# Kernel tuning notes

Hardware: AMD Instinct MI355X
Metric: run time of the kernel (lower is better)

Reference implementation:

```python
import jax, jax.numpy as jnp
import numpy as np

S = 3072       # packed sequence length
DIM = 1280     # hidden dim
H = 16         # num heads
HD = DIM // H  # head dim = 80
NEG = -1e9     # additive mask value for cross-segment entries


def setup_inputs() -> dict:
    key = jax.random.key(0)
    ks = jax.random.split(key, 6)
    x = jax.random.normal(ks[0], (S, DIM), jnp.float32)
    # rope angle table [S, HD//2]
    rotary_pos_emb = jax.random.uniform(ks[1], (S, HD // 2), jnp.float32, 0.0, 2.0 * np.pi)
    # 4 equal image segments packed together
    cu_seqlens = jnp.array([0, 768, 1536, 2304, 3072], jnp.int32)
    w_qkv = jax.random.normal(ks[2], (3 * DIM, DIM), jnp.float32) * 0.02
    b_qkv = jax.random.normal(ks[3], (3 * DIM,), jnp.float32) * 0.02
    w_proj = jax.random.normal(ks[4], (DIM, DIM), jnp.float32) * 0.02
    b_proj = jax.random.normal(ks[5], (DIM,), jnp.float32) * 0.02
    return {"x": x, "cu_seqlens": cu_seqlens, "rotary_pos_emb": rotary_pos_emb,
            "w_qkv": w_qkv, "b_qkv": b_qkv, "w_proj": w_proj, "b_proj": b_proj}


def _rope(t, cos, sin):
    # t: [S, H, HD]; cos/sin: [S, 1, HD]
    t1, t2 = jnp.split(t, 2, axis=-1)
    rot = jnp.concatenate([-t2, t1], axis=-1)
    return t * cos + rot * sin


def reference(x, cu_seqlens, rotary_pos_emb, w_qkv, b_qkv, w_proj, b_proj):
    s, d = x.shape
    qkv = (x @ w_qkv.T + b_qkv).reshape(s, 3, H, HD)
    q, k, v = qkv[:, 0], qkv[:, 1], qkv[:, 2]  # each [S, H, HD]

    # NeoX-style rope with tiled (repeated) freqs, computed in fp32
    cos = jnp.cos(rotary_pos_emb)
    sin = jnp.sin(rotary_pos_emb)
    cos = jnp.concatenate([cos, cos], axis=-1)[:, None, :]  # [S,1,HD]
    sin = jnp.concatenate([sin, sin], axis=-1)[:, None, :]
    q = _rope(q.astype(jnp.float32), cos, sin).astype(x.dtype)
    k = _rope(k.astype(jnp.float32), cos, sin).astype(x.dtype)

    # block-diagonal varlen mask from cu_seqlens: segment id per position
    seg = jnp.searchsorted(cu_seqlens, jnp.arange(s), side='right') - 1  # [S]
    mask = jnp.where(seg[:, None] == seg[None, :], 0.0, NEG).astype(x.dtype)  # [S,S]

    scale = 1.0 / np.sqrt(HD).astype(np.float32)
    scores = jnp.einsum('qhd,khd->hqk', q, k) * scale + mask[None]  # [H,S,S]
    attn = jax.nn.softmax(scores, axis=-1)
    out = jnp.einsum('hqk,khd->qhd', attn, v).reshape(s, d)  # [S, DIM]
    return out @ w_proj.T + b_proj
```

## Files before the change

kernel.cpp:

```cpp
#include <hip/hip_runtime.h>


typedef __bf16 bf16;
typedef __bf16 bf16x4 __attribute__((ext_vector_type(4)));
typedef __bf16 bf16x8 __attribute__((ext_vector_type(8)));
typedef float f32x4 __attribute__((ext_vector_type(4)));
typedef float f32x16 __attribute__((ext_vector_type(16)));
typedef unsigned int u32;

constexpr int S = 3072;
constexpr int DIM = 1280;
constexpr int H = 16;
constexpr int HD = 80;
constexpr int KDP = 128;
constexpr int NQKV = 3 * DIM;

constexpr int MB_A = S / 256;
constexpr int NB_B = NQKV / 256;
constexpr int NKT = DIM / 32;

constexpr float QSCALE = 1.4426950408889634f / 8.94427190999916f;

__device__ __forceinline__ void gload_lds16(const void* g, void* l) {
  __builtin_amdgcn_global_load_lds(
      (const __attribute__((address_space(1))) void*)g,
      (__attribute__((address_space(3))) void*)l, 16, 0, 0);
}

__device__ __forceinline__ u32 pkbf2(float a, float b) {
  union { bf16 h[2]; u32 w; } u;
  u.h[0] = (bf16)a; u.h[1] = (bf16)b;
  return u.w;
}

__device__ __forceinline__ int swv(int s) {
  return ((((s >> 3) & 31) ^ ((s & 7) << 2)) << 2);
}

constexpr long PA_CHUNKS = (long)MB_A * NKT * 1024;
constexpr long PB_CHUNKS = (long)NB_B * NKT * 1024;
constexpr long PW_CHUNKS = (long)DIM * DIM / 8;
constexpr long KP_CHUNKS = (long)H * S * 48 / 8;
constexpr long CS_CHUNKS = (long)S * 40 / 8;
constexpr long TOT_CHUNKS = PA_CHUNKS + PB_CHUNKS + PW_CHUNKS + KP_CHUNKS + CS_CHUNKS;

__global__ __launch_bounds__(256) void pack_inputs(
    const float* __restrict__ x, const float* __restrict__ wq,
    const float* __restrict__ wp, const float* __restrict__ rope,
    bf16* __restrict__ pA, bf16* __restrict__ pB, bf16* __restrict__ wp16,
    bf16* __restrict__ Kb, float* __restrict__ ctab, float* __restrict__ stab) {
  long t = (long)blockIdx.x * 256 + threadIdx.x;
  if (t < PA_CHUNKS + PB_CHUNKS) {
    int blk, rem;
    const float* base;
    bf16* obase;
    bool isB = false;
    if (t < PA_CHUNKS) {
      blk = (int)(t / (NKT * 1024)); rem = (int)(t % (NKT * 1024));
      base = x; obase = pA + t * 8;
    } else {
      long t2 = t - PA_CHUNKS;
      blk = (int)(t2 / (NKT * 1024)); rem = (int)(t2 % (NKT * 1024));
      base = wq; obase = pB + t2 * 8;
      isB = true;
    }
    const int kt = rem >> 10, c = rem & 1023;
    const int lin = c * 16;
    const int logi = lin ^ (((lin >> 7) & 7) << 4);
    int row = logi >> 6;
    const int col = (logi & 63) >> 1;
    int grow = blk * 256 + row;
    if (isB && grow < 2560) {
      const int ty = grow / 1280, rm = grow % 1280;
      const int h = rm / 80, p = rm % 80;
      grow = ty * 1280 + h * 80 + (p >> 1) + (p & 1) * 40;
    }
    const float* src = base + (size_t)grow * DIM + kt * 32 + col;
    float4 v0 = *(const float4*)src;
    float4 v1 = *(const float4*)(src + 4);
    bf16x8 o = {(bf16)v0.x, (bf16)v0.y, (bf16)v0.z, (bf16)v0.w,
                (bf16)v1.x, (bf16)v1.y, (bf16)v1.z, (bf16)v1.w};
    *(bf16x8*)obase = o;
  } else if (t < PA_CHUNKS + PB_CHUNKS + PW_CHUNKS) {
    long t2 = t - PA_CHUNKS - PB_CHUNKS;
    const float* src = wp + t2 * 8;
    float4 v0 = *(const float4*)src;
    float4 v1 = *(const float4*)(src + 4);
    bf16x8 o = {(bf16)v0.x, (bf16)v0.y, (bf16)v0.z, (bf16)v0.w,
                (bf16)v1.x, (bf16)v1.y, (bf16)v1.z, (bf16)v1.w};
    *(bf16x8*)(wp16 + t2 * 8) = o;
  } else if (t < PA_CHUNKS + PB_CHUNKS + PW_CHUNKS + KP_CHUNKS) {
    long t2 = t - PA_CHUNKS - PB_CHUNKS - PW_CHUNKS;
    const int h = (int)(t2 / (S * 6)), r = (int)(t2 % (S * 6));
    const int s = r / 6, cc = r % 6;
    bf16x8 z = {};
    *(bf16x8*)(Kb + ((size_t)h * S + s) * KDP + 80 + cc * 8) = z;
  } else {
    long t3 = t - PA_CHUNKS - PB_CHUNKS - PW_CHUNKS - KP_CHUNKS;
#pragma unroll
    for (int k = 0; k < 8; k++) {
      const int idx = (int)(t3 * 8 + k);
      const int s = idx / 40, a = idx % 40;
      float sn, cs;
      __sincosf(rope[idx], &sn, &cs);
      ctab[a * S + s] = cs;
      stab[a * S + s] = sn;
    }
  }
}

__global__ __launch_bounds__(512, 2) void gemm256(
    const bf16* __restrict__ pA, const bf16* __restrict__ pB,
    const float* __restrict__ bias, const float* __restrict__ ctab,
    const float* __restrict__ stab, bf16* __restrict__ Qb,
    bf16* __restrict__ Kb, bf16* __restrict__ VTb) {
  extern __shared__ char lds[];
  const int tid = threadIdx.x;
  const int w = tid >> 6, lane = tid & 63;
  const int r15 = lane & 15, b4 = lane >> 4;
  const int wr = w >> 2, wc = w & 3;
  const int nwg = gridDim.x * gridDim.y;
  const int orig = blockIdx.y * gridDim.x + blockIdx.x;
  const int xcd = orig % 8, loc = orig / 8;
  const int qq = nwg / 8, rq = nwg % 8;
  const int swzid =
      (xcd < rq ? xcd * (qq + 1) : rq * (qq + 1) + (xcd - rq) * qq) + loc;
  const int nb = swzid % gridDim.x, mb = swzid / gridDim.x;
  const int m0 = mb * 256;
  const char* aPanel = (const char*)pA + (size_t)mb * NKT * 16384;
  const char* bPanel = (const char*)pB + (size_t)nb * NKT * 16384;
  auto stageA = [&](int kt) {
    char* s = lds + (kt & 3) * 32768;
    const char* g = aPanel + (size_t)kt * 16384;
    gload_lds16(g + tid * 16, s + tid * 16);
    gload_lds16(g + 8192 + tid * 16, s + 8192 + tid * 16);
  };
  auto stageB = [&](int kt) {
    char* s = lds + (kt & 3) * 32768 + 16384;
    const char* g = bPanel + (size_t)kt * 16384;
    gload_lds16(g + tid * 16, s + tid * 16);
    gload_lds16(g + 8192 + tid * 16, s + 8192 + tid * 16);
  };
  f32x4 acc[8][4] = {};
  stageA(0); stageB(0); stageA(1); stageB(1); stageA(2); stageB(2);
  asm volatile("s_waitcnt vmcnt(8)" ::: "memory");
  __builtin_amdgcn_s_barrier();
  for (int kt = 0; kt < NKT; ++kt) {
    const char* As = lds + (kt & 3) * 32768;
    const char* Bs = As + 16384;
    const bool pf = (kt + 3 < NKT);
    bf16x8 afr[4], bfr[4];
#pragma unroll
    for (int i = 0; i < 4; i++) {
      int a = (wr * 128 + i * 16 + r15) * 64 + b4 * 16;
      a ^= ((a >> 7) & 7) << 4;
      afr[i] = *(const bf16x8*)(As + a);
    }
#pragma unroll
    for (int j = 0; j < 4; j++) {
      int a = (wc * 64 + j * 16 + r15) * 64 + b4 * 16;
      a ^= ((a >> 7) & 7) << 4;
      bfr[j] = *(const bf16x8*)(Bs + a);
    }
    if (pf) stageA(kt + 3);
    asm volatile("" ::: "memory");
    __builtin_amdgcn_s_barrier();
    __builtin_amdgcn_s_setprio(1);
#pragma unroll
    for (int i = 0; i < 4; i++)
#pragma unroll
      for (int j = 0; j < 4; j++)
        acc[i][j] = __builtin_amdgcn_mfma_f32_16x16x32_bf16(afr[i], bfr[j],
                                                            acc[i][j], 0, 0, 0);
    __builtin_amdgcn_s_setprio(0);
    asm volatile("" ::: "memory");
    __builtin_amdgcn_s_barrier();
#pragma unroll
    for (int i = 0; i < 4; i++) {
      int a = (wr * 128 + 64 + i * 16 + r15) * 64 + b4 * 16;
      a ^= ((a >> 7) & 7) << 4;
      afr[i] = *(const bf16x8*)(As + a);
    }
    if (pf) stageB(kt + 3);
    asm volatile("" ::: "memory");
    __builtin_amdgcn_s_barrier();
    __builtin_amdgcn_s_setprio(1);
#pragma unroll
    for (int i = 0; i < 4; i++)
#pragma unroll
      for (int j = 0; j < 4; j++)
        acc[4 + i][j] = __builtin_amdgcn_mfma_f32_16x16x32_bf16(
            afr[i], bfr[j], acc[4 + i][j], 0, 0, 0);
    __builtin_amdgcn_s_setprio(0);
    const int rem = NKT - 2 - kt;
    if (rem >= 2)      asm volatile("s_waitcnt vmcnt(8)" ::: "memory");
    else if (rem == 1) asm volatile("s_waitcnt vmcnt(4)" ::: "memory");
    else if (rem == 0) asm volatile("s_waitcnt vmcnt(0)" ::: "memory");
    else               asm volatile("" ::: "memory");
    __builtin_amdgcn_s_barrier();
  }
  const int n0 = nb * 256;
  const int type = n0 / 1280;
  const int cpart0 = n0 - type * 1280;
  if (type < 2) {
#pragma unroll
    for (int j = 0; j < 4; j++) {
      const int c = wc * 64 + j * 16 + r15;
      const int cp = cpart0 + c;
      const int h = cp / 80, p = cp % 80;
      const int d = (p >> 1) + (p & 1) * 40;
      const float bv = bias[type * 1280 + h * 80 + d];
      const int a = p >> 1;
#pragma unroll
      for (int i = 0; i < 8; i++) {
        const int sl = wr * 128 + i * 16 + b4 * 4;
        f32x4 cs4 = *(const f32x4*)&ctab[a * S + m0 + sl];
        f32x4 sn4 = *(const f32x4*)&stab[a * S + m0 + sl];
#pragma unroll
        for (int r = 0; r < 4; r++) {
          float v = acc[i][j][r] + bv;
          float ov = __shfl_xor(v, 1);
          float res = (p & 1) ? (v * cs4[r] + ov * sn4[r])
                              : (v * cs4[r] - ov * sn4[r]);
          if (type == 0) res *= QSCALE;
          *(bf16*)(lds + (sl + r) * 512 + ((2 * c) ^ (((sl + r) & 7) << 4))) =
              (bf16)res;
        }
      }
    }
    __syncthreads();
#pragma unroll
    for (int t = 0; t < 16; t++) {
      const int task = t * 512 + tid;
      const int sl = task >> 5, c = (task & 31) * 8;
      bf16x8 v = *(const bf16x8*)(lds + sl * 512 + ((2 * c) ^ ((sl & 7) << 4)));
      const int cp = cpart0 + c, h = cp / 80, p = cp % 80;
      bf16* dst = type ? Kb + ((size_t)h * S + m0 + sl) * KDP + p
                       : Qb + ((size_t)h * S + m0 + sl) * HD + p;
      *(bf16x8*)dst = v;
    }
  } else {
#pragma unroll
    for (int j = 0; j < 4; j++) {
      const int c = wc * 64 + j * 16 + r15;
      const float bv = bias[2560 + cpart0 + c];
#pragma unroll
      for (int i = 0; i < 8; i++) {
        const int sl = wr * 128 + i * 16 + b4 * 4;
#pragma unroll
        for (int r = 0; r < 4; r++) {
          *(bf16*)(lds + (sl + r) * 512 + ((2 * c) ^ swv(sl + r))) =
              (bf16)(acc[i][j][r] + bv);
        }
      }
    }
    __syncthreads();
#pragma unroll
    for (int t = 0; t < 16; t++) {
      const int task = t * 512 + tid;
      const int c = task >> 5, s0 = (task & 31) * 8;
      union { bf16 h[8]; bf16x8 v; } o;
#pragma unroll
      for (int e = 0; e < 8; e++)
        o.h[e] = *(const bf16*)(lds + (s0 + e) * 512 + ((2 * c) ^ swv(s0 + e)));
      const int cp = cpart0 + c, h = cp / 80, d = cp % 80;
      *(bf16x8*)(VTb + ((size_t)(h * 80 + d)) * S + m0 + s0) = o.v;
    }
  }
}

__global__ __launch_bounds__(256) void gemm_proj(
    const bf16* __restrict__ A, const bf16* __restrict__ B,
    const float* __restrict__ bias, float* __restrict__ Cout, int M, int N,
    int K) {
  __shared__ bf16 Al[2][64 * 32];
  __shared__ bf16 Bl[2][128 * 32];
  const int tid = threadIdx.x;
  const int w = tid >> 6, lane = tid & 63;
  const int r15 = lane & 15, b4 = lane >> 4;
  const int nwg = gridDim.x * gridDim.y;
  const int orig = blockIdx.y * gridDim.x + blockIdx.x;
  const int swzid = (orig & 7) * (nwg >> 3) + (orig >> 3);
  const int bx = swzid % gridDim.x, by = swzid / gridDim.x;
  const int m0 = by * 64, n0 = bx * 128;
  const int wm = (w >> 1) * 32, wn = (w & 1) * 64;
  f32x4 acc[2][4] = {};
  const int row0 = tid >> 2, ko0 = (tid & 3) * 8;
  const bf16* Ar = A + (size_t)(m0 + row0) * K + ko0;
  const bf16* Br0 = B + (size_t)(n0 + row0) * K + ko0;
  const bf16* Br1 = B + (size_t)(n0 + row0 + 64) * K + ko0;

  auto stage = [&](int buf, int k0) {
    gload_lds16(Ar + k0, (char*)Al[buf] + tid * 16);
    gload_lds16(Br0 + k0, (char*)Bl[buf] + tid * 16);
    gload_lds16(Br1 + k0, (char*)Bl[buf] + 4096 + tid * 16);
  };

  stage(0, 0);
  int cur = 0;
  for (int k0 = 0; k0 < K; k0 += 32) {
    __syncthreads();
    if (k0 + 32 < K) stage(cur ^ 1, k0 + 32);
    bf16x8 af[2], bfr[4];
#pragma unroll
    for (int i = 0; i < 2; i++)
      af[i] = *(const bf16x8*)((const char*)Al[cur] + (wm + i * 16 + r15) * 64 + b4 * 16);
#pragma unroll
    for (int j = 0; j < 4; j++)
      bfr[j] = *(const bf16x8*)((const char*)Bl[cur] + (wn + j * 16 + r15) * 64 + b4 * 16);
#pragma unroll
    for (int i = 0; i < 2; i++)
#pragma unroll
      for (int j = 0; j < 4; j++)
        acc[i][j] = __builtin_amdgcn_mfma_f32_16x16x32_bf16(af[i], bfr[j], acc[i][j], 0, 0, 0);
    cur ^= 1;
  }
#pragma unroll
  for (int j = 0; j < 4; j++) {
    const int n = n0 + wn + j * 16 + r15;
    const float bv = bias[n];
#pragma unroll
    for (int i = 0; i < 2; i++) {
      const int mr = m0 + wm + i * 16 + b4 * 4;
#pragma unroll
      for (int r = 0; r < 4; r++)
        Cout[(size_t)(mr + r) * N + n] = acc[i][j][r] + bv;
    }
  }
}

__global__ __launch_bounds__(256, 3) void attn_kern(
    const bf16* __restrict__ Qg, const bf16* __restrict__ Kg,
    const bf16* __restrict__ Vg, const int* __restrict__ cu, int nseg,
    bf16* __restrict__ Out) {
  __shared__ bf16 Kl[2][64 * 128];
  __shared__ bf16 Vl[2][80 * 64];
  const int tid = threadIdx.x, w = tid >> 6, lane = tid & 63;
  const int r31 = lane & 31, hi = lane >> 5;
  const int pair = w >> 1, qs = w & 1;
  const int pt = tid & 127;
  const int nwg = gridDim.x;
  const int orig = blockIdx.x;
  const int swzb = (orig & 7) * (nwg >> 3) + (orig >> 3);
  const int h = swzb / 48, qb = swzb % 48;
  const int q = qb * 64 + qs * 32 + r31;
  int sq = 0, eq = S, lo = 0, hik = S;
  {
    const int qlo = qb * 64, qhi = qb * 64 + 63;
#pragma unroll
    for (int i = 0; i < 8; i++) {
      if (i >= nseg) break;
      int a = cu[i], b = cu[i + 1];
      if (q >= a && q < b) { sq = a; eq = b; }
      if (qlo >= a && qlo < b) lo = a;
      if (qhi >= a && qhi < b) hik = b;
    }
  }
  bf16x8 qf[5];
  {
    const bf16* qrow = Qg + ((size_t)h * S + q) * HD + hi * 8;
#pragma unroll
    for (int kk = 0; kk < 5; kk++) qf[kk] = *(const bf16x8*)(qrow + kk * 16);
  }
  int kdst[8], ksrc[8], vdst[5], vsrc[5];
#pragma unroll
  for (int c = 0; c < 8; c++) {
    int lin = (c * 128 + pt) * 16;
    int row = lin >> 8, colb = (lin & 255) ^ ((row & 15) << 4);
    kdst[c] = lin; ksrc[c] = row * KDP + colb / 2;
  }
#pragma unroll
  for (int c = 0; c < 5; c++) {
    int lin = (c * 128 + pt) * 16;
    int row = lin >> 7, colb = (lin & 127) ^ ((row & 7) << 4);
    vdst[c] = lin; vsrc[c] = row * S + colb / 2;
  }
  const bf16* Kbase = Kg + (size_t)h * S * KDP;
  const bf16* Vbase = Vg + (size_t)h * HD * S;
  char* Klp = (char*)Kl[pair];
  char* Vlp = (char*)Vl[pair];
  auto stage = [&](int k0) {
#pragma unroll
    for (int c = 0; c < 8; c++)
      gload_lds16(Kbase + (size_t)k0 * KDP + ksrc[c], Klp + kdst[c]);
#pragma unroll
    for (int c = 0; c < 5; c++)
      gload_lds16(Vbase + vsrc[c] + k0, Vlp + vdst[c]);
  };
  f32x16 o0 = {}, o1 = {}, o2 = {};
  float m = -1e30f, l = 0.f;
  const int nt = (hik - lo) >> 6;
  const int nit = (nt + 1) >> 1;
  for (int i = 0; i < nit; ++i) {
    const int t = 2 * i + pair;
    const bool act = t < nt;
    const int k0 = lo + t * 64;
    __syncthreads();
    if (act) stage(k0);
    asm volatile("s_waitcnt vmcnt(0)" ::: "memory");
    __syncthreads();
    if (!act) continue;
    f32x16 st0 = {}, st1 = {};
    __builtin_amdgcn_s_setprio(1);
#pragma unroll
    for (int kk = 0; kk < 5; kk++) {
      const int colb = kk * 32 + hi * 16;
      bf16x8 kf0 = *(const bf16x8*)(Klp + r31 * 256 + (colb ^ ((r31 & 15) << 4)));
      bf16x8 kf1 = *(const bf16x8*)(Klp + (32 + r31) * 256 + (colb ^ ((r31 & 15) << 4)));
      st0 = __builtin_amdgcn_mfma_f32_32x32x16_bf16(kf0, qf[kk], st0, 0, 0, 0);
      st1 = __builtin_amdgcn_mfma_f32_32x32x16_bf16(kf1, qf[kk], st1, 0, 0, 0);
    }
    __builtin_amdgcn_s_setprio(0);
    float tm = -3e38f;
    if (k0 >= sq && k0 + 63 < eq) {
#pragma unroll
      for (int j = 0; j < 16; j++) {
        tm = fmaxf(tm, st0[j]);
        tm = fmaxf(tm, st1[j]);
      }
    } else {
#pragma unroll
      for (int j = 0; j < 16; j++) {
        const int crow = (j & 3) + 8 * (j >> 2) + 4 * hi;
        int key0 = k0 + crow, key1 = k0 + 32 + crow;
        st0[j] = (key0 >= sq && key0 < eq) ? st0[j] : -1e30f;
        st1[j] = (key1 >= sq && key1 < eq) ? st1[j] : -1e30f;
        tm = fmaxf(tm, st0[j]);
        tm = fmaxf(tm, st1[j]);
      }
    }
    tm = fmaxf(tm, __shfl_xor(tm, 32));
    if (!__all(tm <= m + 8.f)) {
      const float mn = fmaxf(m, tm);
      const float alpha = __builtin_amdgcn_exp2f(m - mn);
      o0 *= alpha; o1 *= alpha; o2 *= alpha;
      l *= alpha;
      m = mn;
    }
    float rs = 0.f;
    u32 wd0[4][2], wd1[4][2];
#pragma unroll
    for (int g2 = 0; g2 < 4; g2++) {
#pragma unroll
      for (int hh = 0; hh < 2; hh++) {
        float a0 = __builtin_amdgcn_exp2f(st0[g2 * 4 + 2 * hh] - m);
        float a1 = __builtin_amdgcn_exp2f(st0[g2 * 4 + 2 * hh + 1] - m);
        float b0 = __builtin_amdgcn_exp2f(st1[g2 * 4 + 2 * hh] - m);
        float b1 = __builtin_amdgcn_exp2f(st1[g2 * 4 + 2 * hh + 1] - m);
        rs += a0 + a1 + b0 + b1;
        wd0[g2][hh] = pkbf2(a0, a1);
        wd1[g2][hh] = pkbf2(b0, b1);
      }
    }
    rs += __shfl_xor(rs, 32);
    l += rs;
    __builtin_amdgcn_s_setprio(1);
#pragma unroll
    for (int kk = 0; kk < 4; kk++) {
      const int g2o = (kk & 1) * 2 + hi;
      const int g2s = (kk & 1) * 2 + (hi ^ 1);
      u32 own0, own1, snd0, snd1;
      if (kk < 2) {
        own0 = wd0[g2o][0]; own1 = wd0[g2o][1];
        snd0 = wd0[g2s][0]; snd1 = wd0[g2s][1];
      } else {
        own0 = wd1[g2o][0]; own1 = wd1[g2o][1];
        snd0 = wd1[g2s][0]; snd1 = wd1[g2s][1];
      }
      u32 rc0 = (u32)__shfl_xor((int)snd0, 32);
      u32 rc1 = (u32)__shfl_xor((int)snd1, 32);
      union { u32 w[4]; bf16x8 v; } pf;
      if (hi == 0) { pf.w[0] = own0; pf.w[1] = own1; pf.w[2] = rc0; pf.w[3] = rc1; }
      else         { pf.w[0] = rc0;  pf.w[1] = rc1;  pf.w[2] = own0; pf.w[3] = own1; }
      const int colb = kk * 32 + hi * 16;
#pragma unroll
      for (int mt = 0; mt < 3; mt++) {
        int row = mt * 32 + r31;
        row = row < HD ? row : 0;
        bf16x8 vf = *(const bf16x8*)(Vlp + row * 128 + (colb ^ ((row & 7) << 4)));
        f32x16* op = mt == 0 ? &o0 : (mt == 1 ? &o1 : &o2);
        *op = __builtin_amdgcn_mfma_f32_32x32x16_bf16(vf, pf.v, *op, 0, 0, 0);
      }
    }
    __builtin_amdgcn_s_setprio(0);
  }
  __syncthreads();
  float* mb = (float*)Kl;
  if (pair == 1) {
    float* d = mb + ((size_t)qs * 64 + lane) * 50;
    d[0] = m; d[1] = l;
#pragma unroll
    for (int j = 0; j < 16; j++) { d[2 + j] = o0[j]; d[18 + j] = o1[j]; d[34 + j] = o2[j]; }
  }
  __syncthreads();
  if (pair == 0) {
    const float* d = mb + ((size_t)qs * 64 + lane) * 50;
    const float pm = d[0], pl = d[1];
    const float mn = fmaxf(m, pm);
    const float a = __builtin_amdgcn_exp2f(m - mn);
    const float b = __builtin_amdgcn_exp2f(pm - mn);
    const float lt = l * a + pl * b;
    const float inv = 1.f / lt;
    bf16* orow = Out + (size_t)q * DIM + h * HD;
#pragma unroll
    for (int rg = 0; rg < 4; rg++) {
      bf16x4 v0, v1;
#pragma unroll
      for (int e = 0; e < 4; e++) {
        v0[e] = (bf16)((o0[rg * 4 + e] * a + d[2 + rg * 4 + e] * b) * inv);
        v1[e] = (bf16)((o1[rg * 4 + e] * a + d[18 + rg * 4 + e] * b) * inv);
      }
      *(bf16x4*)(orow + 8 * rg + 4 * hi) = v0;
      *(bf16x4*)(orow + 32 + 8 * rg + 4 * hi) = v1;
    }
#pragma unroll
    for (int rg = 0; rg < 2; rg++) {
      bf16x4 v2;
#pragma unroll
      for (int e = 0; e < 4; e++)
        v2[e] = (bf16)((o2[rg * 4 + e] * a + d[34 + rg * 4 + e] * b) * inv);
      *(bf16x4*)(orow + 64 + 8 * rg + 4 * hi) = v2;
    }
  }
}

extern "C" void kernel_launch(void* const* d_in, const int* in_sizes, int n_in,
                              void* d_out, int out_size, void* d_ws,
                              size_t ws_size, hipStream_t stream) {
  const float* x = (const float*)d_in[0];
  const int* cu = (const int*)d_in[1];
  const float* rope = (const float*)d_in[2];
  const float* w_qkv = (const float*)d_in[3];
  const float* b_qkv = (const float*)d_in[4];
  const float* w_proj = (const float*)d_in[5];
  const float* b_proj = (const float*)d_in[6];
  const int nseg = in_sizes[1] - 1;

  bf16* pA = (bf16*)d_ws;
  bf16* pB = pA + (size_t)S * DIM;
  bf16* wp16 = pB + (size_t)NQKV * DIM;
  bf16* Qb = wp16 + (size_t)DIM * DIM;
  bf16* Kb = Qb + (size_t)H * S * HD;
  bf16* VTb = Kb + (size_t)H * S * KDP;
  float* ctab = (float*)(VTb + (size_t)H * HD * S);
  float* stab = ctab + (size_t)S * 40;
  bf16* attn16 = pA;

  pack_inputs<<<(int)(TOT_CHUNKS / 256), 256, 0, stream>>>(
      x, w_qkv, w_proj, rope, pA, pB, wp16, Kb, ctab, stab);
  gemm256<<<dim3(NB_B, MB_A), 512, 131072, stream>>>(
      pA, pB, b_qkv, ctab, stab, Qb, Kb, VTb);
  attn_kern<<<H * 48, 256, 0, stream>>>(Qb, Kb, VTb, cu, nseg, attn16);
  gemm_proj<<<dim3(DIM / 128, S / 64), 256, 0, stream>>>(
      attn16, wp16, b_proj, (float*)d_out, S, DIM, DIM);
}
```

Baseline: 118.9 us.

## Shrink QKV GEMM M-tile to 192 rows to raise workgroup count

```diff
diff --git a/kernel.cpp b/kernel.cpp
--- a/kernel.cpp
+++ b/kernel.cpp
@@ -15,9 +15,12 @@
 constexpr int KDP = 128;
 constexpr int NQKV = 3 * DIM;
 
-constexpr int MB_A = S / 256;
+constexpr int BM = 192;
+constexpr int MB_A = S / BM;
 constexpr int NB_B = NQKV / 256;
 constexpr int NKT = DIM / 32;
+constexpr int ASL = BM * 32 * 2;
+constexpr int SLOT = ASL + 16384;
 
 constexpr float QSCALE = 1.4426950408889634f / 8.94427190999916f;
 
@@ -37,7 +40,7 @@
   return ((((s >> 3) & 31) ^ ((s & 7) << 2)) << 2);
 }
 
-constexpr long PA_CHUNKS = (long)MB_A * NKT * 1024;
+constexpr long PA_CHUNKS = (long)MB_A * NKT * (ASL / 16);
 constexpr long PB_CHUNKS = (long)NB_B * NKT * 1024;
 constexpr long PW_CHUNKS = (long)DIM * DIM / 8;
 constexpr long KP_CHUNKS = (long)H * S * 48 / 8;
@@ -50,37 +53,37 @@
     bf16* __restrict__ pA, bf16* __restrict__ pB, bf16* __restrict__ wp16,
     bf16* __restrict__ Kb, float* __restrict__ ctab, float* __restrict__ stab) {
   long t = (long)blockIdx.x * 256 + threadIdx.x;
-  if (t < PA_CHUNKS + PB_CHUNKS) {
-    int blk, rem;
-    const float* base;
-    bf16* obase;
-    bool isB = false;
-    if (t < PA_CHUNKS) {
-      blk = (int)(t / (NKT * 1024)); rem = (int)(t % (NKT * 1024));
-      base = x; obase = pA + t * 8;
-    } else {
-      long t2 = t - PA_CHUNKS;
-      blk = (int)(t2 / (NKT * 1024)); rem = (int)(t2 % (NKT * 1024));
-      base = wq; obase = pB + t2 * 8;
-      isB = true;
-    }
-    const int kt = rem >> 10, c = rem & 1023;
+  if (t < PA_CHUNKS) {
+    const int blk = (int)(t / (NKT * 768)), rem = (int)(t % (NKT * 768));
+    const int kt = rem / 768, c = rem - kt * 768;
     const int lin = c * 16;
     const int logi = lin ^ (((lin >> 7) & 7) << 4);
-    int row = logi >> 6;
-    const int col = (logi & 63) >> 1;
-    int grow = blk * 256 + row;
-    if (isB && grow < 2560) {
-      const int ty = grow / 1280, rm = grow % 1280;
-      const int h = rm / 80, p = rm % 80;
-      grow = ty * 1280 + h * 80 + (p >> 1) + (p & 1) * 40;
-    }
-    const float* src = base + (size_t)grow * DIM + kt * 32 + col;
+    const int row = logi >> 6, col = (logi & 63) >> 1;
+    const float* src = x + (size_t)(blk * BM + row) * DIM + kt * 32 + col;
     float4 v0 = *(const float4*)src;
     float4 v1 = *(const float4*)(src + 4);
     bf16x8 o = {(bf16)v0.x, (bf16)v0.y, (bf16)v0.z, (bf16)v0.w,
                 (bf16)v1.x, (bf16)v1.y, (bf16)v1.z, (bf16)v1.w};
-    *(bf16x8*)obase = o;
+    *(bf16x8*)(pA + t * 8) = o;
+  } else if (t < PA_CHUNKS + PB_CHUNKS) {
+    long t2 = t - PA_CHUNKS;
+    const int blk = (int)(t2 / (NKT * 1024)), rem = (int)(t2 % (NKT * 1024));
+    const int kt = rem >> 10, c = rem & 1023;
+    const int lin = c * 16;
+    const int logi = lin ^ (((lin >> 7) & 7) << 4);
+    const int row = logi >> 6, col = (logi & 63) >> 1;
+    int grow = blk * 256 + row;
+    if (grow < 2560) {
+      const int ty = grow / 1280, rm = grow % 1280;
+      const int h = rm / 80, p = rm % 80;
+      grow = ty * 1280 + h * 80 + (p >> 1) + (p & 1) * 40;
+    }
+    const float* src = wq + (size_t)grow * DIM + kt * 32 + col;
+    float4 v0 = *(const float4*)src;
+    float4 v1 = *(const float4*)(src + 4);
+    bf16x8 o = {(bf16)v0.x, (bf16)v0.y, (bf16)v0.z, (bf16)v0.w,
+                (bf16)v1.x, (bf16)v1.y, (bf16)v1.z, (bf16)v1.w};
+    *(bf16x8*)(pB + t2 * 8) = o;
   } else if (t < PA_CHUNKS + PB_CHUNKS + PW_CHUNKS) {
     long t2 = t - PA_CHUNKS - PB_CHUNKS;
     const float* src = wp + t2 * 8;
@@ -126,33 +129,35 @@
   const int swzid =
       (xcd < rq ? xcd * (qq + 1) : rq * (qq + 1) + (xcd - rq) * qq) + loc;
   const int nb = swzid % gridDim.x, mb = swzid / gridDim.x;
-  const int m0 = mb * 256;
-  const char* aPanel = (const char*)pA + (size_t)mb * NKT * 16384;
+  const int m0 = mb * BM;
+  const char* aPanel = (const char*)pA + (size_t)mb * NKT * ASL;
   const char* bPanel = (const char*)pB + (size_t)nb * NKT * 16384;
   auto stageA = [&](int kt) {
-    char* s = lds + (kt & 3) * 32768;
-    const char* g = aPanel + (size_t)kt * 16384;
+    char* s = lds + (kt & 3) * SLOT;
+    const char* g = aPanel + (size_t)kt * ASL;
     gload_lds16(g + tid * 16, s + tid * 16);
-    gload_lds16(g + 8192 + tid * 16, s + 8192 + tid * 16);
+    if (tid < 256)
+      gload_lds16(g + 8192 + tid * 16, s + 8192 + tid * 16);
   };
   auto stageB = [&](int kt) {
-    char* s = lds + (kt & 3) * 32768 + 16384;
+    char* s = lds + (kt & 3) * SLOT + ASL;
     const char* g = bPanel + (size_t)kt * 16384;
     gload_lds16(g + tid * 16, s + tid * 16);
     gload_lds16(g + 8192 + tid * 16, s + 8192 + tid * 16);
   };
-  f32x4 acc[8][4] = {};
+  f32x4 acc[6][4] = {};
   stageA(0); stageB(0); stageA(1); stageB(1); stageA(2); stageB(2);
-  asm volatile("s_waitcnt vmcnt(8)" ::: "memory");
+  if (tid < 256) asm volatile("s_waitcnt vmcnt(8)" ::: "memory");
+  else           asm volatile("s_waitcnt vmcnt(6)" ::: "memory");
   __builtin_amdgcn_s_barrier();
   for (int kt = 0; kt < NKT; ++kt) {
-    const char* As = lds + (kt & 3) * 32768;
-    const char* Bs = As + 16384;
+    const char* As = lds + (kt & 3) * SLOT;
+    const char* Bs = As + ASL;
     const bool pf = (kt + 3 < NKT);
-    bf16x8 afr[4], bfr[4];
-#pragma unroll
-    for (int i = 0; i < 4; i++) {
-      int a = (wr * 128 + i * 16 + r15) * 64 + b4 * 16;
+    bf16x8 afr[3], bfr[4];
+#pragma unroll
+    for (int i = 0; i < 3; i++) {
+      int a = (wr * 96 + i * 16 + r15) * 64 + b4 * 16;
       a ^= ((a >> 7) & 7) << 4;
       afr[i] = *(const bf16x8*)(As + a);
     }
@@ -167,7 +172,7 @@
     __builtin_amdgcn_s_barrier();
     __builtin_amdgcn_s_setprio(1);
 #pragma unroll
-    for (int i = 0; i < 4; i++)
+    for (int i = 0; i < 3; i++)
 #pragma unroll
       for (int j = 0; j < 4; j++)
         acc[i][j] = __builtin_amdgcn_mfma_f32_16x16x32_bf16(afr[i], bfr[j],
@@ -176,8 +181,8 @@
     asm volatile("" ::: "memory");
     __builtin_amdgcn_s_barrier();
 #pragma unroll
-    for (int i = 0; i < 4; i++) {
-      int a = (wr * 128 + 64 + i * 16 + r15) * 64 + b4 * 16;
+    for (int i = 0; i < 3; i++) {
+      int a = (wr * 96 + 48 + i * 16 + r15) * 64 + b4 * 16;
       a ^= ((a >> 7) & 7) << 4;
       afr[i] = *(const bf16x8*)(As + a);
     }
@@ -186,17 +191,24 @@
     __builtin_amdgcn_s_barrier();
     __builtin_amdgcn_s_setprio(1);
 #pragma unroll
-    for (int i = 0; i < 4; i++)
+    for (int i = 0; i < 3; i++)
 #pragma unroll
       for (int j = 0; j < 4; j++)
-        acc[4 + i][j] = __builtin_amdgcn_mfma_f32_16x16x32_bf16(
-            afr[i], bfr[j], acc[4 + i][j], 0, 0, 0);
+        acc[3 + i][j] = __builtin_amdgcn_mfma_f32_16x16x32_bf16(
+            afr[i], bfr[j], acc[3 + i][j], 0, 0, 0);
     __builtin_amdgcn_s_setprio(0);
     const int rem = NKT - 2 - kt;
-    if (rem >= 2)      asm volatile("s_waitcnt vmcnt(8)" ::: "memory");
-    else if (rem == 1) asm volatile("s_waitcnt vmcnt(4)" ::: "memory");
-    else if (rem == 0) asm volatile("s_waitcnt vmcnt(0)" ::: "memory");
-    else               asm volatile("" ::: "memory");
+    if (tid < 256) {
+      if (rem >= 2)      asm volatile("s_waitcnt vmcnt(8)" ::: "memory");
+      else if (rem == 1) asm volatile("s_waitcnt vmcnt(4)" ::: "memory");
+      else if (rem == 0) asm volatile("s_waitcnt vmcnt(0)" ::: "memory");
+      else               asm volatile("" ::: "memory");
+    } else {
+      if (rem >= 2)      asm volatile("s_waitcnt vmcnt(6)" ::: "memory");
+      else if (rem == 1) asm volatile("s_waitcnt vmcnt(3)" ::: "memory");
+      else if (rem == 0) asm volatile("s_waitcnt vmcnt(0)" ::: "memory");
+      else               asm volatile("" ::: "memory");
+    }
     __builtin_amdgcn_s_barrier();
   }
   const int n0 = nb * 256;
@@ -212,8 +224,8 @@
       const float bv = bias[type * 1280 + h * 80 + d];
       const int a = p >> 1;
 #pragma unroll
-      for (int i = 0; i < 8; i++) {
-        const int sl = wr * 128 + i * 16 + b4 * 4;
+      for (int i = 0; i < 6; i++) {
+        const int sl = wr * 96 + i * 16 + b4 * 4;
         f32x4 cs4 = *(const f32x4*)&ctab[a * S + m0 + sl];
         f32x4 sn4 = *(const f32x4*)&stab[a * S + m0 + sl];
 #pragma unroll
@@ -230,7 +242,7 @@
     }
     __syncthreads();
 #pragma unroll
-    for (int t = 0; t < 16; t++) {
+    for (int t = 0; t < 12; t++) {
       const int task = t * 512 + tid;
       const int sl = task >> 5, c = (task & 31) * 8;
       bf16x8 v = *(const bf16x8*)(lds + sl * 512 + ((2 * c) ^ ((sl & 7) << 4)));
@@ -245,8 +257,8 @@
       const int c = wc * 64 + j * 16 + r15;
       const float bv = bias[2560 + cpart0 + c];
 #pragma unroll
-      for (int i = 0; i < 8; i++) {
-        const int sl = wr * 128 + i * 16 + b4 * 4;
+      for (int i = 0; i < 6; i++) {
+        const int sl = wr * 96 + i * 16 + b4 * 4;
 #pragma unroll
         for (int r = 0; r < 4; r++) {
           *(bf16*)(lds + (sl + r) * 512 + ((2 * c) ^ swv(sl + r))) =
@@ -256,9 +268,9 @@
     }
     __syncthreads();
 #pragma unroll
-    for (int t = 0; t < 16; t++) {
+    for (int t = 0; t < 12; t++) {
       const int task = t * 512 + tid;
-      const int c = task >> 5, s0 = (task & 31) * 8;
+      const int c = task & 255, s0 = (task >> 8) * 8;
       union { bf16 h[8]; bf16x8 v; } o;
 #pragma unroll
       for (int e = 0; e < 8; e++)
@@ -548,7 +560,7 @@
 
   pack_inputs<<<(int)(TOT_CHUNKS / 256), 256, 0, stream>>>(
       x, w_qkv, w_proj, rope, pA, pB, wp16, Kb, ctab, stab);
-  gemm256<<<dim3(NB_B, MB_A), 512, 131072, stream>>>(
+  gemm256<<<dim3(NB_B, MB_A), 512, 114688, stream>>>(
       pA, pB, b_qkv, ctab, stab, Qb, Kb, VTb);
   attn_kern<<<H * 48, 256, 0, stream>>>(Qb, Kb, VTb, cu, nseg, attn16);
   gemm_proj<<<dim3(DIM / 128, S / 64), 256, 0, stream>>>(
```

Result: faster. 111.4 us (-6.4%).
